# Optimization experiments

Measured on AMD Instinct MI355X. Metric: run time of the kernel, lower is better.

The kernel has to match this reference:

```python
import jax, jax.numpy as jnp
import numpy as np

B, T_PREFIX, C_IN = 8, 6144, 8
OUT_LEN, OUT_C = 2048, 8
AUX_DIM = 16
D_MODEL, D_STATE, HEADDIM, EXPAND = 256, 32, 64, 2
D_INNER = EXPAND * D_MODEL            # 512
NHEADS = D_INNER // HEADDIM           # 8
CONV_DIM = D_INNER + 2 * D_STATE      # 576
D_PROJ = 2 * D_INNER + 2 * D_STATE + NHEADS  # 1096
N_LAYERS = 2
CHUNK = 64
PATCH = 16
PRECONV_K = 5
DCONV_K = 4


def setup_inputs() -> dict:
    key = jax.random.key(0)
    ks = iter(jax.random.split(key, 64))
    def rn(shape, s=0.02):
        return s * jax.random.normal(next(ks), shape, jnp.float32)
    inp = dict(
        x_prefix=jax.random.normal(next(ks), (B, T_PREFIX, C_IN), jnp.float32),
        y_aux=jax.random.normal(next(ks), (B, AUX_DIM), jnp.float32),
        pre_conv_w=rn((D_MODEL, C_IN, PRECONV_K), 0.1),
        pre_conv_b=rn((D_MODEL,)),
        patch_w=rn((D_MODEL, D_MODEL, PATCH), 0.05),
        patch_b=rn((D_MODEL,)),
        mask_token=rn((D_MODEL,)),
        aux_w=rn((AUX_DIM, D_MODEL), 0.1),
        aux_b=rn((D_MODEL,)),
        patch_out_w=rn((2 * D_MODEL, OUT_C * PATCH), 0.05),
        patch_out_b=rn((OUT_C * PATCH,)),
    )
    for d in ('fwd', 'bwd'):
        inp[f'{d}_norm_w'] = jnp.ones((N_LAYERS, D_MODEL), jnp.float32)
        inp[f'{d}_inproj'] = rn((N_LAYERS, D_MODEL, D_PROJ), 0.05)
        inp[f'{d}_conv_w'] = rn((N_LAYERS, CONV_DIM, DCONV_K), 0.2)
        inp[f'{d}_conv_b'] = rn((N_LAYERS, CONV_DIM))
        inp[f'{d}_dtbias'] = rn((N_LAYERS, NHEADS), 0.5)
        inp[f'{d}_Alog'] = jnp.tile(jnp.log(jnp.arange(1, NHEADS + 1, dtype=jnp.float32)), (N_LAYERS, 1))
        inp[f'{d}_D'] = jnp.ones((N_LAYERS, NHEADS), jnp.float32)
        inp[f'{d}_gnorm'] = jnp.ones((N_LAYERS, D_INNER), jnp.float32)
        inp[f'{d}_outproj'] = rn((N_LAYERS, D_INNER, D_MODEL), 0.05)
    return inp


def rmsnorm(x, w, eps=1e-5):
    return x * jax.lax.rsqrt(jnp.mean(x * x, axis=-1, keepdims=True) + eps) * w


def conv1d(x, w, b, stride, pad):  # x: [B,C,T], w: [O,I,K]
    y = jax.lax.conv_general_dilated(x, w, (stride,), [(pad, pad)],
                                     dimension_numbers=('NCH', 'OIH', 'NCH'))
    return y + b[None, :, None]


def mamba_block(u, inproj, conv_w, conv_b, dtbias, Alog, Dp, gnorm_w, outproj):
    # Mamba-2/SSD style block: in_proj -> z | xBC | dt, causal depthwise conv,
    # selective scan with per-head scalar decay A, +D skip, gated RMSNorm, out_proj.
    b, T, _ = u.shape
    zxbcdt = u @ inproj                                   # [b,T,D_PROJ]
    z = zxbcdt[..., :D_INNER]
    xBC = zxbcdt[..., D_INNER:D_INNER + CONV_DIM]
    dt = jax.nn.softplus(zxbcdt[..., -NHEADS:] + dtbias)  # [b,T,H]
    # causal depthwise conv over time
    xc = jax.lax.conv_general_dilated(xBC.transpose(0, 2, 1), conv_w[:, None, :], (1,),
                                      [(DCONV_K - 1, 0)],
                                      dimension_numbers=('NCH', 'OIH', 'NCH'),
                                      feature_group_count=CONV_DIM)
    xBC = jax.nn.silu((xc + conv_b[None, :, None]).transpose(0, 2, 1))
    xs = xBC[..., :D_INNER].reshape(b, T, NHEADS, HEADDIM)  # [b,T,H,P]
    Bm = xBC[..., D_INNER:D_INNER + D_STATE]                # [b,T,N]
    Cm = xBC[..., D_INNER + D_STATE:]                       # [b,T,N]
    A = -jnp.exp(Alog)                                      # [H]

    def step(h, inps):  # h: [b,H,P,N]
        dt_t, x_t, B_t, C_t = inps
        dA = jnp.exp(dt_t * A)[:, :, None, None]
        h = h * dA + (dt_t[:, :, None] * x_t)[..., None] * B_t[:, None, None, :]
        y = jnp.einsum('bhpn,bn->bhp', h, C_t)
        return h, y

    h0 = jnp.zeros((b, NHEADS, HEADDIM, D_STATE), u.dtype)
    _, ys = jax.lax.scan(step, h0, (dt.transpose(1, 0, 2), xs.transpose(1, 0, 2, 3),
                                    Bm.transpose(1, 0, 2), Cm.transpose(1, 0, 2)))
    y = ys.transpose(1, 0, 2, 3) + Dp[None, None, :, None] * xs
    y = y.reshape(b, T, D_INNER)
    y = rmsnorm(y * jax.nn.silu(z), gnorm_w)
    return y @ outproj


def reference(x_prefix, y_aux, pre_conv_w, pre_conv_b, patch_w, patch_b, mask_token,
              aux_w, aux_b, fwd_norm_w, fwd_inproj, fwd_conv_w, fwd_conv_b, fwd_dtbias,
              fwd_Alog, fwd_D, fwd_gnorm, fwd_outproj, bwd_norm_w, bwd_inproj,
              bwd_conv_w, bwd_conv_b, bwd_dtbias, bwd_Alog, bwd_D, bwd_gnorm,
              bwd_outproj, patch_out_w, patch_out_b):
    b = x_prefix.shape[0]
    t_total = T_PREFIX + OUT_LEN
    x_full = jnp.pad(x_prefix, ((0, 0), (0, OUT_LEN), (0, 0)))        # zeros for future
    x = jax.nn.silu(conv1d(x_full.transpose(0, 2, 1), pre_conv_w, pre_conv_b, 1, PRECONV_K // 2))
    x = conv1d(x, patch_w, patch_b, PATCH, 0).transpose(0, 2, 1)      # [b, n_tokens, d_model]
    n_tokens = x.shape[1]
    # eval mode: deterministic future-patch mask, dropout is identity
    starts = jnp.arange(n_tokens) * PATCH
    mask = (starts >= T_PREFIX)[None, :, None]
    x = jnp.where(mask, mask_token[None, None, :], x)
    aux_bias = jax.nn.silu(y_aux @ aux_w + aux_b)[:, None, :]
    x = x + aux_bias
    pad_t = (-n_tokens) % CHUNK
    if pad_t:
        x = jnp.pad(x, ((0, 0), (0, pad_t), (0, 0)))
    h_f = x
    h_b = x[:, ::-1]
    for i in range(N_LAYERS):
        h_f = h_f + mamba_block(rmsnorm(h_f, fwd_norm_w[i]), fwd_inproj[i], fwd_conv_w[i],
                                fwd_conv_b[i], fwd_dtbias[i], fwd_Alog[i], fwd_D[i],
                                fwd_gnorm[i], fwd_outproj[i])
        h_b = h_b + mamba_block(rmsnorm(h_b, bwd_norm_w[i]), bwd_inproj[i], bwd_conv_w[i],
                                bwd_conv_b[i], bwd_dtbias[i], bwd_Alog[i], bwd_D[i],
                                bwd_gnorm[i], bwd_outproj[i])
    h = jnp.concatenate([h_f, h_b[:, ::-1]], axis=-1)[:, :n_tokens]   # [b,n,2*d_model]
    patch_pred = h @ patch_out_w + patch_out_b                        # [b,n,out_c*patch]
    y = patch_pred.reshape(b, n_tokens, OUT_C, PATCH).reshape(b, n_tokens * PATCH, OUT_C)
    y = y[:, :t_total, :]
    return y[:, T_PREFIX:, :]
```

## Files before the change

### kernel.cpp

```cpp
#include <hip/hip_runtime.h>
#include <hip/hip_bf16.h>
#include <math.h>

#define BSZ      8
#define TPREF    6144
#define CIN      8
#define DMODEL   256
#define DINNER   512
#define DSTATE   32
#define NHEADS   8
#define HEADDIM  64
#define CONVDIM  576
#define DPROJ    1096
#define ZXW      1088
#define NTOK     512
#define NVIS     384
#define TBWD     128
#define MFWD     (BSZ * NTOK)
#define MBWD     (BSZ * TBWD)
#define MALL     (MFWD + MBWD)

typedef float f32x4 __attribute__((ext_vector_type(4)));
typedef __bf16 bf16x8 __attribute__((ext_vector_type(8)));

// ... 28 lines not shown
        for (int i = 0; i < 2; i++) {
            int s = i * 256 + tid;
            ASYNC16(A + (size_t)(m0 + (s >> 2)) * K + kb + (s & 3) * 8, sm + s * 16);
        }
        #pragma unroll
        for (int i = 0; i < 2; i++) {
            int s = i * 256 + tid;
            ASYNC16(Bt + (size_t)(n0 + (s >> 2)) * K + kb + (s & 3) * 8, sm + 8192 + s * 16);
        }
        __syncthreads();
        bf16x8 af[4], bfr[4];
        #pragma unroll
        for (int mf = 0; mf < 4; mf++)
            af[mf] = *(const bf16x8*)(sm + (wm * 64 + mf * 16 + lm) * 64 + q * 16);
        #pragma unroll
        for (int nf = 0; nf < 4; nf++)
            bfr[nf] = *(const bf16x8*)(sm + 8192 + (wn * 64 + nf * 16 + lm) * 64 + q * 16);
        #pragma unroll
        for (int mf = 0; mf < 4; mf++)
            #pragma unroll
            for (int nf = 0; nf < 4; nf++)
                acc[mf][nf] = __builtin_amdgcn_mfma_f32_16x16x32_bf16(af[mf], bfr[nf], acc[mf][nf], 0, 0, 0);
        __syncthreads();
    }

    #pragma unroll
    for (int mf = 0; mf < 4; mf++) {
        int mbase = m0 + wm * 64 + mf * 16 + q * 4;
        #pragma unroll
        for (int nf = 0; nf < 4; nf++) {
            int n = n0 + wn * 64 + nf * 16 + lm;
            if (n < N) {
                #pragma unroll
                for (int r = 0; r < 4; r++) {
                    float v = acc[mf][nf][r];
                    if (flags & 4) {
                        v = silu_f(v + bias[n]);
                        ((__bf16*)C)[(size_t)(mbase + r) * ldc + n] = (__bf16)v;
                    } else if (flags & 16) {
                        int mm = mbase + r;
                        int bb = mm / NVIS, tk = mm - bb * NVIS;
                        atomicAdd(C + ((size_t)(bb * NTOK + tk)) * 256 + n, v);
                    } else if (flags & 2) {
                        atomicAdd(C + (size_t)(mbase + r) * ldc + n, v);
                    } else {
                        C[(size_t)(mbase + r) * ldc + n] = v;
                    }
                }
            }
        }
    }
}

__global__ __launch_bounds__(256) void final_gemm(
    const float* __restrict__ h_all, const __bf16* __restrict__ poT,
    float* __restrict__ out) {
    __shared__ __bf16 Asm_[128][40];
    __shared__ char Bsm[8192];
    int tid = threadIdx.x;
    int m0 = blockIdx.y * 128;
    int z = blockIdx.z;
    int w = tid >> 6, l = tid & 63;
    int wm = w >> 1, wn_ = w & 1, lm = l & 15, q = l >> 4;
    f32x4 acc[4][4];
    #pragma unroll
    for (int i = 0; i < 4; i++)
        #pragma unroll
        for (int j = 0; j < 4; j++) acc[i][j] = (f32x4)0.f;

    int r = tid >> 1, half = tid & 1;
    int m = m0 + r;
    int b = m >> 7, jj = m & 127;
    size_t arow = (z == 0) ? ((size_t)(b * NTOK + NVIS + jj) * 256)
                           : ((size_t)MFWD * 256 + (size_t)(b * TBWD + (TBWD - 1 - jj)) * 256);
    for (int k0 = 0; k0 < 256; k0 += 32) {
        {
            const float4* sp = (const float4*)(h_all + arow + k0 + half * 16);
            float4 v0 = sp[0], v1 = sp[1], v2 = sp[2], v3 = sp[3];
            union { uint4 u; __bf16 hh[8]; } d0, d1;
            d0.hh[0] = (__bf16)v0.x; d0.hh[1] = (__bf16)v0.y; d0.hh[2] = (__bf16)v0.z; d0.hh[3] = (__bf16)v0.w;
            d0.hh[4] = (__bf16)v1.x; d0.hh[5] = (__bf16)v1.y; d0.hh[6] = (__bf16)v1.z; d0.hh[7] = (__bf16)v1.w;
            d1.hh[0] = (__bf16)v2.x; d1.hh[1] = (__bf16)v2.y; d1.hh[2] = (__bf16)v2.z; d1.hh[3] = (__bf16)v2.w;
            d1.hh[4] = (__bf16)v3.x; d1.hh[5] = (__bf16)v3.y; d1.hh[6] = (__bf16)v3.z; d1.hh[7] = (__bf16)v3.w;
            *(uint4*)&Asm_[r][half * 16] = d0.u;
            *(uint4*)&Asm_[r][half * 16 + 8] = d1.u;
        }
        #pragma unroll
        for (int i = 0; i < 2; i++) {
            int s = i * 256 + tid;
            ASYNC16(poT + (size_t)(s >> 2) * 512 + z * 256 + k0 + (s & 3) * 8, Bsm + s * 16);
        }
        __syncthreads();
        bf16x8 af[4], bfr[4];
        #pragma unroll
        for (int mf = 0; mf < 4; mf++)
            af[mf] = *(const bf16x8*)&Asm_[wm * 64 + mf * 16 + lm][q * 8];
        #pragma unroll
        for (int nf = 0; nf < 4; nf++)
            bfr[nf] = *(const bf16x8*)(Bsm + (wn_ * 64 + nf * 16 + lm) * 64 + q * 16);
        #pragma unroll
        for (int mf = 0; mf < 4; mf++)
            #pragma unroll
            for (int nf = 0; nf < 4; nf++)
                acc[mf][nf] = __builtin_amdgcn_mfma_f32_16x16x32_bf16(af[mf], bfr[nf], acc[mf][nf], 0, 0, 0);
        __syncthreads();
    }
    #pragma unroll
    for (int mf = 0; mf < 4; mf++) {
        int mbase = m0 + wm * 64 + mf * 16 + q * 4;
        #pragma unroll
        for (int nf = 0; nf < 4; nf++) {
            int n = wn_ * 64 + nf * 16 + lm;
            #pragma unroll
            for (int rr = 0; rr < 4; rr++)
                atomicAdd(out + (size_t)(mbase + rr) * 128 + n, acc[mf][nf][rr]);
        }
    }
}

__global__ __launch_bounds__(256) void gemm_inproj(
    const __bf16* __restrict__ u, const __bf16* __restrict__ ipTf,
    const __bf16* __restrict__ ipTb, __bf16* __restrict__ zxb, float* __restrict__ dtc) {
    __shared__ char sm[16384];
    int tid = threadIdx.x;
    int m0 = blockIdx.y * 128, n0 = blockIdx.x * 128;
    const __bf16* Bt = (m0 >= MFWD) ? ipTb : ipTf;
    int w = tid >> 6, l = tid & 63;
    int wm = w >> 1, wn = w & 1, lm = l & 15, q = l >> 4;
    f32x4 acc[4][4];
    #pragma unroll
    for (int i = 0; i < 4; i++)
        #pragma unroll
        for (int j = 0; j < 4; j++) acc[i][j] = (f32x4)0.f;
    for (int k0 = 0; k0 < 256; k0 += 32) {
        #pragma unroll
        for (int i = 0; i < 2; i++) {
            int s = i * 256 + tid;
            ASYNC16(u + (size_t)(m0 + (s >> 2)) * 256 + k0 + (s & 3) * 8, sm + s * 16);
        }
        #pragma unroll
        for (int i = 0; i < 2; i++) {
            int s = i * 256 + tid;
            ASYNC16(Bt + (size_t)(n0 + (s >> 2)) * 256 + k0 + (s & 3) * 8, sm + 8192 + s * 16);
// ... 88 lines not shown
}

__global__ __launch_bounds__(256) void rmsnorm_all(
    const float* __restrict__ h, const float* __restrict__ wf,
    const float* __restrict__ wb, __bf16* __restrict__ u) {
    int row = blockIdx.x * 4 + (threadIdx.x >> 6);
    int lane = threadIdx.x & 63;
    const float* w = (row >= MFWD) ? wb : wf;
    float4 v = ((const float4*)(h + (size_t)row * 256))[lane];
    float ss = v.x * v.x + v.y * v.y + v.z * v.z + v.w * v.w;
    #pragma unroll
    for (int off = 32; off >= 1; off >>= 1) ss += __shfl_xor(ss, off);
    float rs = rsqrtf(ss * (1.f / 256.f) + 1e-5f);
    float4 wv = ((const float4*)w)[lane];
    __bf16 o4[4] = {(__bf16)(v.x * rs * wv.x), (__bf16)(v.y * rs * wv.y),
                    (__bf16)(v.z * rs * wv.z), (__bf16)(v.w * rs * wv.w)};
    *(uint2*)(u + (size_t)row * 256 + lane * 4) = *(uint2*)o4;
}

__global__ __launch_bounds__(256) void gatednorm_all(
    const __bf16* __restrict__ ysD, const __bf16* __restrict__ zxb,
    const float* __restrict__ gwf, const float* __restrict__ gwb,
    __bf16* __restrict__ y2) {
    int row = blockIdx.x * 4 + (threadIdx.x >> 6);
    int lane = threadIdx.x & 63;
    const float* gw = (row >= MFWD) ? gwb : gwf;
    union { uint4 u; __bf16 hh[8]; } yv, zv;
    yv.u = *(const uint4*)(ysD + (size_t)row * 512 + lane * 8);
    zv.u = *(const uint4*)(zxb + (size_t)row * ZXW + lane * 8);
    float g[8];
    #pragma unroll
    for (int j = 0; j < 8; j++) g[j] = (float)yv.hh[j] * silu_f((float)zv.hh[j]);
    float ss = 0.f;
    #pragma unroll
    for (int j = 0; j < 8; j++) ss += g[j] * g[j];
    #pragma unroll
    for (int off = 32; off >= 1; off >>= 1) ss += __shfl_xor(ss, off);
    float rs = rsqrtf(ss * (1.f / 512.f) + 1e-5f);
    const float4* gr = (const float4*)(gw + lane * 8);
    float4 g0 = gr[0], g1 = gr[1];
    union { uint4 u; __bf16 hh[8]; } d;
    d.hh[0] = (__bf16)(g[0] * rs * g0.x); d.hh[1] = (__bf16)(g[1] * rs * g0.y);
    d.hh[2] = (__bf16)(g[2] * rs * g0.z); d.hh[3] = (__bf16)(g[3] * rs * g0.w);
    d.hh[4] = (__bf16)(g[4] * rs * g1.x); d.hh[5] = (__bf16)(g[5] * rs * g1.y);
    d.hh[6] = (__bf16)(g[6] * rs * g1.z); d.hh[7] = (__bf16)(g[7] * rs * g1.w);
    *(uint4*)(y2 + (size_t)row * 512 + lane * 8) = d.u;
}

__global__ void prep_all(const float* __restrict__ pre_conv_w, const float* __restrict__ patch_w,
                         const float* __restrict__ ip0, const float* __restrict__ ip1,
                         const float* __restrict__ op0, const float* __restrict__ op1,
                         const float* __restrict__ pow_, const float* __restrict__ pob,
                         const float* __restrict__ y_aux, const float* __restrict__ aux_w,
                         const float* __restrict__ aux_b, const float* __restrict__ xp,
                         const float* __restrict__ patch_b, const float* __restrict__ mtok,
                         __bf16* __restrict__ WpreT, __bf16* __restrict__ WtT,
                         __bf16* __restrict__ inprojT, __bf16* __restrict__ outprojT,
                         __bf16* __restrict__ poT, float* __restrict__ dout,
                         __bf16* __restrict__ Aim, float* __restrict__ h_all) {
    __shared__ float tile[32][33];
    int bx = blockIdx.x, tid = threadIdx.x;
    int tx = tid & 31, ty = tid >> 5;
    if (bx < 256) {
        int o = bx, c = tid;
        float f[16];
        const float4* s = (const float4*)(patch_w + (size_t)o * 4096 + c * 16);
        #pragma unroll
        for (int j = 0; j < 4; j++) *(float4*)&f[j * 4] = s[j];
        #pragma unroll
        for (int k = 0; k < 16; k++)
            WtT[(size_t)o * 4096 + k * 256 + c] = (__bf16)f[k];
        return;
    }
    bx -= 256;
    if (bx < 1152) {
        int seg = bx / 288, rem = bx % 288;
        int n0 = (rem / 8) * 32, k0 = (rem % 8) * 32;
        const float* src = (seg < 2 ? ip0 : ip1) + (size_t)(seg & 1) * 256 * DPROJ;
        #pragma unroll
        for (int j = 0; j < 4; j++) {
            int r = ty + j * 8;
            int n = n0 + tx;
            tile[r][tx] = (n < DPROJ) ? src[(size_t)(k0 + r) * DPROJ + n] : 0.f;
        }
        __syncthreads();
        __bf16* dst = inprojT + (size_t)seg * 1152 * 256;
        #pragma unroll
        for (int j = 0; j < 4; j++) {
            int r = ty + j * 8;
            dst[(size_t)(n0 + r) * 256 + k0 + tx] = (__bf16)tile[tx][r];
        }
        return;
    }
    bx -= 1152;
    if (bx < 512) {
        int s = bx / 128, rem = bx % 128;
        int n0 = (rem / 16) * 32, k0 = (rem % 16) * 32;
        const float* src = (s < 2 ? op0 : op1) + (size_t)(s & 1) * DINNER * DMODEL;
        #pragma unroll
        for (int j = 0; j < 4; j++) {
            int r = ty + j * 8;
            tile[r][tx] = src[(size_t)(k0 + r) * 256 + n0 + tx];
        }
        __syncthreads();
        __bf16* dst = outprojT + (size_t)s * 256 * 512;
        #pragma unroll
        for (int j = 0; j < 4; j++) {
            int r = ty + j * 8;
            dst[(size_t)(n0 + r) * 512 + k0 + tx] = (__bf16)tile[tx][r];
        }
        return;
    }
    bx -= 512;
    if (bx < 64) {
        int n0 = (bx / 16) * 32, k0 = (bx % 16) * 32;
        #pragma unroll
        for (int j = 0; j < 4; j++) {
            int r = ty + j * 8;
            tile[r][tx] = pow_[(size_t)(k0 + r) * 128 + n0 + tx];
        }
        __syncthreads();
        #pragma unroll
        for (int j = 0; j < 4; j++) {
            int r = ty + j * 8;
            poT[(size_t)(n0 + r) * 512 + k0 + tx] = (__bf16)tile[tx][r];
        }
        return;
    }
    bx -= 64;
    if (bx < 64) {
        int idx = bx * 256 + tid;
        int o = idx >> 6, kk = idx & 63;
        WpreT[idx] = (kk < 40) ? (__bf16)pre_conv_w[o * 40 + kk] : (__bf16)0.f;
        return;
    }
    bx -= 64;
    if (bx < 512) {
        int idx = bx * 256 + tid;
        dout[idx] = pob[idx & 127];
        return;
    }
    bx -= 512;
    if (bx < 192) {
        int m = bx * 256 + tid;
        int t = m % TPREF, b = m / TPREF;
        __bf16 d[64];
        #pragma unroll
        for (int k = 0; k < 5; k++) {
            int tt = t - 2 + k;
            bool ok = (tt >= 0) && (tt < TPREF);
            const float* s = xp + ((size_t)b * TPREF + tt) * 8;
            #pragma unroll
            for (int i = 0; i < 8; i++)
                d[i * 5 + k] = ok ? (__bf16)s[i] : (__bf16)0.f;
        }
        #pragma unroll
        for (int j = 40; j < 64; j++) d[j] = (__bf16)0.f;
        uint4* o = (uint4*)(Aim + (size_t)m * 64);
        #pragma unroll
        for (int k = 0; k < 8; k++) o[k] = ((const uint4*)d)[k];
        return;
    }
    bx -= 192;
    {
        int row = bx, o = tid;
        int b; bool masked;
        if (row < MFWD) { b = row >> 9; int tok = row & 511; masked = (tok >= NVIS); }
        else { b = (row - MFWD) >> 7; masked = true; }
        float acc = aux_b[o];
        #pragma unroll
        for (int i = 0; i < 16; i++) acc += y_aux[b * 16 + i] * aux_w[i * 256 + o];
        float v = (masked ? mtok[o] : patch_b[o]) + silu_f(acc);
        h_all[(size_t)row * 256 + o] = v;
    }
}

__global__ __launch_bounds__(256) void dwconv2_kernel(
    const __bf16* __restrict__ zxb, const float* __restrict__ cwf, const float* __restrict__ cbf,
    const float* __restrict__ cwb, const float* __restrict__ cbb,
    __bf16* __restrict__ XtF, __bf16* __restrict__ XtB,
    __bf16* __restrict__ BCF, __bf16* __restrict__ BCB) {
    int cg = blockIdx.x;
    int id = blockIdx.y;
    int b, t0, T; size_t rowbase;
    const float *cw, *cb; __bf16 *Xt, *BC;
    if (id < 64) { b = id >> 3; t0 = (id & 7) * 64; T = NTOK; rowbase = (size_t)b * NTOK;
                   cw = cwf; cb = cbf; Xt = XtF; BC = BCF; }
    else { int i2 = id - 64; b = i2 >> 1; t0 = (i2 & 1) * 64; T = TBWD;
           rowbase = (size_t)MFWD + (size_t)b * TBWD; cw = cwb; cb = cbb; Xt = XtB; BC = BCB; }
    int c0 = cg * 64;
    __shared__ float xs[67][65];
    int lane = threadIdx.x & 63, grp = threadIdx.x >> 6;
    for (int r = grp; r < 67; r += 4) {
        int t = t0 - 3 + r;
        xs[r][lane] = (t >= 0) ? (float)zxb[(rowbase + t) * ZXW + DINNER + c0 + lane] : 0.f;
    }
    __syncthreads();
    if (cg < 8) {
        int t = lane;
        #pragma unroll
        for (int ci = grp; ci < 64; ci += 4) {
            int c = c0 + ci;
            float acc = cb[c];
            #pragma unroll
            for (int k = 0; k < 4; k++) acc += cw[c * 4 + k] * xs[t + k][ci];
            Xt[((size_t)((b * 8 + cg) * 64 + ci)) * T + t0 + t] = (__bf16)silu_f(acc);
        }
    } else {
        int c = lane;
        #pragma unroll
        for (int ti = grp; ti < 64; ti += 4) {
            float acc = cb[c0 + c];
            #pragma unroll
            for (int k = 0; k < 4; k++) acc += cw[(c0 + c) * 4 + k] * xs[ti + k][c];
            BC[((size_t)(b * T + t0 + ti)) * 64 + c] = (__bf16)silu_f(acc);
        }
    }
}

__global__ __launch_bounds__(64) void scan_local(
    const __bf16* __restrict__ XtF, const __bf16* __restrict__ XtB,
    const __bf16* __restrict__ BCF, const __bf16* __restrict__ BCB,
    const float* __restrict__ dtc,
    const float* __restrict__ dtbf, const float* __restrict__ dtbb,
    const float* __restrict__ Alogf, const float* __restrict__ Alogb,
    const float* __restrict__ Dpf, const float* __restrict__ Dpb,
    __bf16* __restrict__ ysD,
    __bf16* __restrict__ ChatF, __bf16* __restrict__ ChatB,
    float* __restrict__ dSF, float* __restrict__ dSB,
    float* __restrict__ DcsF, float* __restrict__ DcsB, int layer) {
    int id = blockIdx.x, hd = blockIdx.y;
    int b, c, T, NC; size_t rowbase;
    const __bf16 *Xt, *BC; __bf16* Chat; float *dS, *Dcs;
    const float *dtb, *Alog, *Dp;
    if (id < 64) { b = id >> 3; c = id & 7; T = NTOK; NC = 8; rowbase = (size_t)b * NTOK;
                   Xt = XtF; BC = BCF; Chat = ChatF; dS = dSF; Dcs = DcsF;
                   dtb = dtbf; Alog = Alogf; Dp = Dpf; }
    else { int i2 = id - 64; b = i2 >> 1; c = i2 & 1; T = TBWD; NC = 2;
           rowbase = (size_t)MFWD + (size_t)b * TBWD;
           Xt = XtB; BC = BCB; Chat = ChatB; dS = dSB; Dcs = DcsB;
           dtb = dtbb; Alog = Alogb; Dp = Dpb; }
    bool skipY = (layer == 1) && (id < 64) && (c < 6);
    int bh = b * 8 + hd;
    int t0 = c * 64;
    int lane = threadIdx.x;
    int lm = lane & 15, q = lane >> 4;
    float A = -expf(Alog[hd]);
    float Dh = Dp[hd];

    __shared__ char smem[23552];
    __bf16 (*Xl)[72]  = (__bf16(*)[72])(smem);
    __bf16 (*BCl)[72] = (__bf16(*)[72])(smem + 9216);
    __bf16 (*Pl)[72]  = (__bf16(*)[72])(smem + 9216);
    __bf16 (*Wbl)[72] = (__bf16(*)[72])(smem + 18432);
    float* lcs = (float*)(smem + 23040);
    float* dts = (float*)(smem + 23296);

    const uint4* xg = (const uint4*)(Xt + (size_t)(bh * 64 + lane) * T + t0);
    const uint4* bg = (const uint4*)(BC + ((size_t)(b * T + t0 + lane)) * 64);
    uint4 xv[8], bv[8];
    #pragma unroll
    for (int k = 0; k < 8; k++) { xv[k] = xg[k]; bv[k] = bg[k]; }
    float xdt = dtc[(rowbase + t0 + lane) * 8 + hd] + dtb[hd];
    float dtv = (xdt > 20.f) ? xdt : log1pf(expf(xdt));
    #pragma unroll
    for (int k = 0; k < 8; k++) {
        *(uint4*)&Xl[lane][k * 8] = xv[k];
        if (!skipY) *(uint4*)&BCl[lane][k * 8] = bv[k];
    }
    float lc = A * dtv;
    #pragma unroll
    for (int off = 1; off < 64; off <<= 1) {
        float o = __shfl_up(lc, off);
        if (lane >= off) lc += o;
    }
    lcs[lane] = lc; dts[lane] = dtv;
    float lc63 = __shfl(lc, 63);
    float wj = expf(lc63 - lc) * dtv;
    float eli = expf(lc);
    float Dc = expf(lc63);
    if (lane == 0) Dcs[bh * NC + c] = Dc;
    if (!skipY) {
        __bf16* co = Chat + ((size_t)(bh * NC + c) * 64 + lane) * 32;
        #pragma unroll
        for (int k = 0; k < 4; k++) {
            union { uint4 u; __bf16 h[8]; } s; s.u = bv[4 + k];
            union { uint4 u; __bf16 h[8]; } d;
            #pragma unroll
            for (int j = 0; j < 8; j++) d.h[j] = (__bf16)(eli * (float)s.h[j]);
            *(uint4*)(co + k * 8) = d.u;
        }
    }
    #pragma unroll
    for (int k = 0; k < 4; k++) {
        union { uint4 u; __bf16 h[8]; } s; s.u = bv[k];
        #pragma unroll
        for (int j = 0; j < 8; j++) Wbl[k * 8 + j][lane] = (__bf16)(wj * (float)s.h[j]);
    }
    __syncthreads();

    bf16x8 xf0[4], xf1[4];
    if (!skipY) {
        bf16x8 cfr[4], bfr[4];
        #pragma unroll
        for (int t4 = 0; t4 < 4; t4++) {
            cfr[t4] = *(const bf16x8*)&BCl[t4 * 16 + lm][32 + q * 8];
            bfr[t4] = *(const bf16x8*)&BCl[t4 * 16 + lm][q * 8];
        }
        #pragma unroll
        for (int ti = 0; ti < 4; ti++) {
            float lci[4];
            #pragma unroll
            for (int r = 0; r < 4; r++) lci[r] = lcs[ti * 16 + q * 4 + r];
            #pragma unroll
            for (int tj = 0; tj < 4; tj++) {
                if (tj > ti) {
                    #pragma unroll
                    for (int r = 0; r < 4; r++) Pl[ti * 16 + q * 4 + r][tj * 16 + lm] = (__bf16)0.f;
                    continue;
                }
                f32x4 g = __builtin_amdgcn_mfma_f32_16x16x32_bf16(cfr[ti], bfr[tj], (f32x4)0.f, 0, 0, 0);
                int j = tj * 16 + lm;
                float lcj = lcs[j], dtj = dts[j];
                #pragma unroll
                for (int r = 0; r < 4; r++) {
                    int i = ti * 16 + q * 4 + r;
                    float v = (j <= i) ? g[r] * expf(lci[r] - lcj) * dtj : 0.f;
                    if (j == i) v += Dh;
                    Pl[i][j] = (__bf16)v;
                }
            }
        }
        __syncthreads();

// ... 88 lines not shown
    int w = tid >> 6, l = tid & 63, lm = l & 15, q = l >> 4;
    for (int c = cmin + w; c < NC; c += 4) {
        int t0 = c * 64;
        const __bf16* Cb = Chat + (size_t)(bh * NC + c) * 2048;
        bf16x8 cf[4], sf[4];
        #pragma unroll
        for (int t4 = 0; t4 < 4; t4++) {
            cf[t4] = *(const bf16x8*)(Cb + (t4 * 16 + lm) * 32 + q * 8);
            sf[t4] = *(const bf16x8*)&Spl[c][t4 * 16 + lm][q * 8];
        }
        #pragma unroll
        for (int ti = 0; ti < 4; ti++) {
            #pragma unroll
            for (int tp = 0; tp < 4; tp++) {
                f32x4 y = __builtin_amdgcn_mfma_f32_16x16x32_bf16(cf[ti], sf[tp], (f32x4)0.f, 0, 0, 0);
                #pragma unroll
                for (int r = 0; r < 4; r++) {
                    int i = ti * 16 + q * 4 + r;
                    size_t idx = (rowbase + t0 + i) * DINNER + hd * 64 + tp * 16 + lm;
                    ysD[idx] = (__bf16)((float)ysD[idx] + y[r]);
                }
            }
        }
    }
}

extern "C" void kernel_launch(void* const* d_in, const int* in_sizes, int n_in,
                              void* d_out, int out_size, void* d_ws, size_t ws_size,
                              hipStream_t stream) {
    const float* x_prefix    = (const float*)d_in[0];
    const float* y_aux       = (const float*)d_in[1];
    const float* pre_conv_w  = (const float*)d_in[2];
    const float* pre_conv_b  = (const float*)d_in[3];
    const float* patch_w     = (const float*)d_in[4];
    const float* patch_b     = (const float*)d_in[5];
    const float* mask_token  = (const float*)d_in[6];
    const float* aux_w       = (const float*)d_in[7];
    const float* aux_b       = (const float*)d_in[8];
    const float* patch_out_w = (const float*)d_in[9];
    const float* patch_out_b = (const float*)d_in[10];
    const float* w_norm[2]   = {(const float*)d_in[11], (const float*)d_in[20]};
    const float* w_inproj[2] = {(const float*)d_in[12], (const float*)d_in[21]};
    const float* w_convw[2]  = {(const float*)d_in[13], (const float*)d_in[22]};
    const float* w_convb[2]  = {(const float*)d_in[14], (const float*)d_in[23]};
    const float* w_dtb[2]    = {(const float*)d_in[15], (const float*)d_in[24]};
    const float* w_alog[2]   = {(const float*)d_in[16], (const float*)d_in[25]};
    const float* w_D[2]      = {(const float*)d_in[17], (const float*)d_in[26]};
    const float* w_gnorm[2]  = {(const float*)d_in[18], (const float*)d_in[27]};
    const float* w_outproj[2]= {(const float*)d_in[19], (const float*)d_in[28]};

    char* p = (char*)d_ws;
    auto alloc = [&](size_t bytes) { char* r = p; p += (bytes + 255) & ~255ULL; return r; };
    __bf16* A_patch  = (__bf16*)alloc((size_t)3072 * 4096 * 2);
    __bf16* Aim      = (__bf16*)alloc((size_t)BSZ * TPREF * 64 * 2);
    __bf16* WpreT    = (__bf16*)alloc((size_t)256 * 64 * 2);
    __bf16* WtT      = (__bf16*)alloc((size_t)256 * 4096 * 2);
    __bf16* inprojT  = (__bf16*)alloc((size_t)4 * 1152 * 256 * 2);
    __bf16* outprojT = (__bf16*)alloc((size_t)4 * 256 * 512 * 2);
    __bf16* poT      = (__bf16*)alloc((size_t)128 * 512 * 2);
    float*  h_all    = (float*)alloc((size_t)MALL * 256 * 4);
    __bf16* u        = (__bf16*)alloc((size_t)MALL * 256 * 2);
    __bf16* zxb      = (__bf16*)alloc((size_t)MALL * ZXW * 2);
    float*  dtc      = (float*)alloc((size_t)MALL * 8 * 4);
    __bf16* XtF      = (__bf16*)alloc((size_t)64 * 64 * NTOK * 2);
    __bf16* XtB      = (__bf16*)alloc((size_t)64 * 64 * TBWD * 2);
    __bf16* BCF      = (__bf16*)alloc((size_t)BSZ * NTOK * 64 * 2);
    __bf16* BCB      = (__bf16*)alloc((size_t)BSZ * TBWD * 64 * 2);
    __bf16* ysD      = (__bf16*)alloc((size_t)MALL * DINNER * 2);
    __bf16* y2       = (__bf16*)alloc((size_t)MALL * DINNER * 2);
    __bf16* ChatF    = (__bf16*)alloc((size_t)64 * 8 * 2048 * 2);
    __bf16* ChatB    = (__bf16*)alloc((size_t)64 * 2 * 2048 * 2);
    float*  dSF      = (float*)alloc((size_t)64 * 8 * 2048 * 4);
    float*  dSB      = (float*)alloc((size_t)64 * 2 * 2048 * 4);
    float*  DcsF     = (float*)alloc((size_t)64 * 8 * 4);
    float*  DcsB     = (float*)alloc((size_t)64 * 2 * 4);

    prep_all<<<256 + 1152 + 512 + 64 + 64 + 512 + 192 + MALL, 256, 0, stream>>>(
        pre_conv_w, patch_w, w_inproj[0], w_inproj[1], w_outproj[0], w_outproj[1],
        patch_out_w, patch_out_b, y_aux, aux_w, aux_b, x_prefix, patch_b, mask_token,
        WpreT, WtT, inprojT, outprojT, poT, (float*)d_out, Aim, h_all);
    gemm_mfma<<<dim3(2, (BSZ * TPREF) / 128, 1), 256, 0, stream>>>(
        Aim, WpreT, (float*)A_patch, pre_conv_b, 256, 64, 256, 4);
    gemm_mfma<<<dim3(2, 24, 8), 256, 0, stream>>>(
        A_patch, WtT, h_all, nullptr, 256, 4096, 256, 16);

    for (int i = 0; i < 2; i++) {
        const __bf16* ipTf = inprojT + (size_t)(0 * 2 + i) * 1152 * 256;
        const __bf16* ipTb = inprojT + (size_t)(1 * 2 + i) * 1152 * 256;
        const __bf16* opTf = outprojT + (size_t)(0 * 2 + i) * 256 * 512;
        const __bf16* opTb = outprojT + (size_t)(1 * 2 + i) * 256 * 512;
        rmsnorm_all<<<MALL / 4, 256, 0, stream>>>(h_all, w_norm[0] + i * 256, w_norm[1] + i * 256, u);
        gemm_inproj<<<dim3(9, MALL / 128), 256, 0, stream>>>(u, ipTf, ipTb, zxb, dtc);
        dwconv2_kernel<<<dim3(9, 80), 256, 0, stream>>>(
            zxb, w_convw[0] + i * CONVDIM * 4, w_convb[0] + i * CONVDIM,
            w_convw[1] + i * CONVDIM * 4, w_convb[1] + i * CONVDIM,
            XtF, XtB, BCF, BCB);
        scan_local<<<dim3(80, NHEADS), 64, 0, stream>>>(
            XtF, XtB, BCF, BCB, dtc,
            w_dtb[0] + i * 8, w_dtb[1] + i * 8,
            w_alog[0] + i * 8, w_alog[1] + i * 8,
            w_D[0] + i * 8, w_D[1] + i * 8,
            ysD, ChatF, ChatB, dSF, dSB, DcsF, DcsB, i);
        scan_tail<<<128, 256, 0, stream>>>(dSF, dSB, DcsF, DcsB, ChatF, ChatB, ysD, i);
        gatednorm_all<<<MALL / 4, 256, 0, stream>>>(
            ysD, zxb, w_gnorm[0] + i * DINNER, w_gnorm[1] + i * DINNER, y2);
        int oy = (i == 0) ? (MALL / 128) : 16;
        gemm_outproj<<<dim3(2, oy), 256, 0, stream>>>(y2, opTf, opTb, h_all, i);
    }

    final_gemm<<<dim3(1, 8, 2), 256, 0, stream>>>(h_all, poT, (float*)d_out);
}
```

Measured before the change: 338.2 us.

## Fuse im2col into preconv GEMM, depthwise conv into scan, split final GEMM K

```diff
diff --git a/kernel.cpp b/kernel.cpp
--- a/kernel.cpp
+++ b/kernel.cpp
@@ -104,6 +104,78 @@
     }
 }
 
+__global__ __launch_bounds__(256) void preconv_gemm(
+    const float* __restrict__ xp, const __bf16* __restrict__ WpreT,
+    const float* __restrict__ bias, __bf16* __restrict__ Apatch) {
+    __shared__ char sm[32768];
+    int tid = threadIdx.x;
+    int m0 = blockIdx.y * 128, n0 = blockIdx.x * 128;
+    int w = tid >> 6, l = tid & 63;
+    int wm = w >> 1, wn = w & 1, lm = l & 15, q = l >> 4;
+
+    #pragma unroll
+    for (int i = 0; i < 4; i++) {
+        int s = i * 256 + tid;
+        int kh = s >> 9, row = (s & 511) >> 2, within = s & 3;
+        ASYNC16(WpreT + (size_t)(n0 + row) * 64 + kh * 32 + within * 8, sm + 16384 + s * 16);
+    }
+    if (tid < 128) {
+        int m = m0 + tid;
+        int b = m / TPREF, t = m - b * TPREF;
+        __bf16 d[64];
+        #pragma unroll
+        for (int j = 40; j < 64; j++) d[j] = (__bf16)0.f;
+        #pragma unroll
+        for (int k = 0; k < 5; k++) {
+            int tt = t - 2 + k;
+            bool ok = (tt >= 0) && (tt < TPREF);
+            const float* s = xp + ((size_t)b * TPREF + tt) * 8;
+            #pragma unroll
+            for (int i = 0; i < 8; i++)
+                d[i * 5 + k] = ok ? (__bf16)s[i] : (__bf16)0.f;
+        }
+        uint4* o0 = (uint4*)(sm + tid * 64);
+        uint4* o1 = (uint4*)(sm + 8192 + tid * 64);
+        #pragma unroll
+        for (int k = 0; k < 4; k++) { o0[k] = ((const uint4*)d)[k]; o1[k] = ((const uint4*)d)[4 + k]; }
+    }
+    __syncthreads();
+
+    f32x4 acc[4][4];
+    #pragma unroll
+    for (int i = 0; i < 4; i++)
+        #pragma unroll
+        for (int j = 0; j < 4; j++) acc[i][j] = (f32x4)0.f;
+    #pragma unroll
+    for (int kh = 0; kh < 2; kh++) {
+        bf16x8 af[4], bfr[4];
+        #pragma unroll
+        for (int mf = 0; mf < 4; mf++)
+            af[mf] = *(const bf16x8*)(sm + kh * 8192 + (wm * 64 + mf * 16 + lm) * 64 + q * 16);
+        #pragma unroll
+        for (int nf = 0; nf < 4; nf++)
+            bfr[nf] = *(const bf16x8*)(sm + 16384 + kh * 8192 + (wn * 64 + nf * 16 + lm) * 64 + q * 16);
+        #pragma unroll
+        for (int mf = 0; mf < 4; mf++)
+            #pragma unroll
+            for (int nf = 0; nf < 4; nf++)
+                acc[mf][nf] = __builtin_amdgcn_mfma_f32_16x16x32_bf16(af[mf], bfr[nf], acc[mf][nf], 0, 0, 0);
+    }
+    #pragma unroll
+    for (int mf = 0; mf < 4; mf++) {
+        int mbase = m0 + wm * 64 + mf * 16 + q * 4;
+        #pragma unroll
+        for (int nf = 0; nf < 4; nf++) {
+            int n = n0 + wn * 64 + nf * 16 + lm;
+            #pragma unroll
+            for (int r = 0; r < 4; r++) {
+                float v = silu_f(acc[mf][nf][r] + bias[n]);
+                Apatch[(size_t)(mbase + r) * 256 + n] = (__bf16)v;
+            }
+        }
+    }
+}
+
 __global__ __launch_bounds__(256) void final_gemm(
     const float* __restrict__ h_all, const __bf16* __restrict__ poT,
     float* __restrict__ out) {
@@ -112,6 +184,8 @@
     int tid = threadIdx.x;
     int m0 = blockIdx.y * 128;
     int z = blockIdx.z;
+    int dir = z >> 1, kh = z & 1;
+    int koff = kh * 128;
     int w = tid >> 6, l = tid & 63;
     int wm = w >> 1, wn_ = w & 1, lm = l & 15, q = l >> 4;
     f32x4 acc[4][4];
@@ -123,11 +197,11 @@
     int r = tid >> 1, half = tid & 1;
     int m = m0 + r;
     int b = m >> 7, jj = m & 127;
-    size_t arow = (z == 0) ? ((size_t)(b * NTOK + NVIS + jj) * 256)
-                           : ((size_t)MFWD * 256 + (size_t)(b * TBWD + (TBWD - 1 - jj)) * 256);
-    for (int k0 = 0; k0 < 256; k0 += 32) {
+    size_t arow = (dir == 0) ? ((size_t)(b * NTOK + NVIS + jj) * 256)
+                             : ((size_t)MFWD * 256 + (size_t)(b * TBWD + (TBWD - 1 - jj)) * 256);
+    for (int k0 = 0; k0 < 128; k0 += 32) {
         {
-            const float4* sp = (const float4*)(h_all + arow + k0 + half * 16);
+            const float4* sp = (const float4*)(h_all + arow + koff + k0 + half * 16);
             float4 v0 = sp[0], v1 = sp[1], v2 = sp[2], v3 = sp[3];
             union { uint4 u; __bf16 hh[8]; } d0, d1;
             d0.hh[0] = (__bf16)v0.x; d0.hh[1] = (__bf16)v0.y; d0.hh[2] = (__bf16)v0.z; d0.hh[3] = (__bf16)v0.w;
@@ -140,7 +214,7 @@
         #pragma unroll
         for (int i = 0; i < 2; i++) {
             int s = i * 256 + tid;
-            ASYNC16(poT + (size_t)(s >> 2) * 512 + z * 256 + k0 + (s & 3) * 8, Bsm + s * 16);
+            ASYNC16(poT + (size_t)(s >> 2) * 512 + dir * 256 + koff + k0 + (s & 3) * 8, Bsm + s * 16);
         }
         __syncthreads();
         bf16x8 af[4], bfr[4];
@@ -335,12 +409,12 @@
                          const float* __restrict__ op0, const float* __restrict__ op1,
                          const float* __restrict__ pow_, const float* __restrict__ pob,
                          const float* __restrict__ y_aux, const float* __restrict__ aux_w,
-                         const float* __restrict__ aux_b, const float* __restrict__ xp,
+                         const float* __restrict__ aux_b,
                          const float* __restrict__ patch_b, const float* __restrict__ mtok,
                          __bf16* __restrict__ WpreT, __bf16* __restrict__ WtT,
                          __bf16* __restrict__ inprojT, __bf16* __restrict__ outprojT,
                          __bf16* __restrict__ poT, float* __restrict__ dout,
-                         __bf16* __restrict__ Aim, float* __restrict__ h_all) {
+                         float* __restrict__ h_all) {
     __shared__ float tile[32][33];
     int bx = blockIdx.x, tid = threadIdx.x;
     int tx = tid & 31, ty = tid >> 5;
@@ -424,27 +498,6 @@
         return;
     }
     bx -= 512;
-    if (bx < 192) {
-        int m = bx * 256 + tid;
-        int t = m % TPREF, b = m / TPREF;
-        __bf16 d[64];
-        #pragma unroll
-        for (int k = 0; k < 5; k++) {
-            int tt = t - 2 + k;
-            bool ok = (tt >= 0) && (tt < TPREF);
-            const float* s = xp + ((size_t)b * TPREF + tt) * 8;
-            #pragma unroll
-            for (int i = 0; i < 8; i++)
-                d[i * 5 + k] = ok ? (__bf16)s[i] : (__bf16)0.f;
-        }
-        #pragma unroll
-        for (int j = 40; j < 64; j++) d[j] = (__bf16)0.f;
-        uint4* o = (uint4*)(Aim + (size_t)m * 64);
-        #pragma unroll
-        for (int k = 0; k < 8; k++) o[k] = ((const uint4*)d)[k];
-        return;
-    }
-    bx -= 192;
     {
         int row = bx, o = tid;
         int b; bool masked;
@@ -458,52 +511,10 @@
     }
 }
 
-__global__ __launch_bounds__(256) void dwconv2_kernel(
-    const __bf16* __restrict__ zxb, const float* __restrict__ cwf, const float* __restrict__ cbf,
+__global__ __launch_bounds__(64) void scan_local(
+    const __bf16* __restrict__ zxb,
+    const float* __restrict__ cwf, const float* __restrict__ cbf,
     const float* __restrict__ cwb, const float* __restrict__ cbb,
-    __bf16* __restrict__ XtF, __bf16* __restrict__ XtB,
-    __bf16* __restrict__ BCF, __bf16* __restrict__ BCB) {
-    int cg = blockIdx.x;
-    int id = blockIdx.y;
-    int b, t0, T; size_t rowbase;
-    const float *cw, *cb; __bf16 *Xt, *BC;
-    if (id < 64) { b = id >> 3; t0 = (id & 7) * 64; T = NTOK; rowbase = (size_t)b * NTOK;
-                   cw = cwf; cb = cbf; Xt = XtF; BC = BCF; }
-    else { int i2 = id - 64; b = i2 >> 1; t0 = (i2 & 1) * 64; T = TBWD;
-           rowbase = (size_t)MFWD + (size_t)b * TBWD; cw = cwb; cb = cbb; Xt = XtB; BC = BCB; }
-    int c0 = cg * 64;
-    __shared__ float xs[67][65];
-    int lane = threadIdx.x & 63, grp = threadIdx.x >> 6;
-    for (int r = grp; r < 67; r += 4) {
-        int t = t0 - 3 + r;
-        xs[r][lane] = (t >= 0) ? (float)zxb[(rowbase + t) * ZXW + DINNER + c0 + lane] : 0.f;
-    }
-    __syncthreads();
-    if (cg < 8) {
-        int t = lane;
-        #pragma unroll
-        for (int ci = grp; ci < 64; ci += 4) {
-            int c = c0 + ci;
-            float acc = cb[c];
-            #pragma unroll
-            for (int k = 0; k < 4; k++) acc += cw[c * 4 + k] * xs[t + k][ci];
-            Xt[((size_t)((b * 8 + cg) * 64 + ci)) * T + t0 + t] = (__bf16)silu_f(acc);
-        }
-    } else {
-        int c = lane;
-        #pragma unroll
-        for (int ti = grp; ti < 64; ti += 4) {
-            float acc = cb[c0 + c];
-            #pragma unroll
-            for (int k = 0; k < 4; k++) acc += cw[(c0 + c) * 4 + k] * xs[ti + k][c];
-            BC[((size_t)(b * T + t0 + ti)) * 64 + c] = (__bf16)silu_f(acc);
-        }
-    }
-}
-
-__global__ __launch_bounds__(64) void scan_local(
-    const __bf16* __restrict__ XtF, const __bf16* __restrict__ XtB,
-    const __bf16* __restrict__ BCF, const __bf16* __restrict__ BCB,
     const float* __restrict__ dtc,
     const float* __restrict__ dtbf, const float* __restrict__ dtbb,
     const float* __restrict__ Alogf, const float* __restrict__ Alogb,
@@ -514,15 +525,15 @@
     float* __restrict__ DcsF, float* __restrict__ DcsB, int layer) {
     int id = blockIdx.x, hd = blockIdx.y;
     int b, c, T, NC; size_t rowbase;
-    const __bf16 *Xt, *BC; __bf16* Chat; float *dS, *Dcs;
-    const float *dtb, *Alog, *Dp;
+    __bf16* Chat; float *dS, *Dcs;
+    const float *dtb, *Alog, *Dp, *cw, *cb;
     if (id < 64) { b = id >> 3; c = id & 7; T = NTOK; NC = 8; rowbase = (size_t)b * NTOK;
-                   Xt = XtF; BC = BCF; Chat = ChatF; dS = dSF; Dcs = DcsF;
-                   dtb = dtbf; Alog = Alogf; Dp = Dpf; }
+                   Chat = ChatF; dS = dSF; Dcs = DcsF;
+                   dtb = dtbf; Alog = Alogf; Dp = Dpf; cw = cwf; cb = cbf; }
     else { int i2 = id - 64; b = i2 >> 1; c = i2 & 1; T = TBWD; NC = 2;
            rowbase = (size_t)MFWD + (size_t)b * TBWD;
-           Xt = XtB; BC = BCB; Chat = ChatB; dS = dSB; Dcs = DcsB;
-           dtb = dtbb; Alog = Alogb; Dp = Dpb; }
+           Chat = ChatB; dS = dSB; Dcs = DcsB;
+           dtb = dtbb; Alog = Alogb; Dp = Dpb; cw = cwb; cb = cbb; }
     bool skipY = (layer == 1) && (id < 64) && (c < 6);
     int bh = b * 8 + hd;
     int t0 = c * 64;
@@ -531,26 +542,60 @@
     float A = -expf(Alog[hd]);
     float Dh = Dp[hd];
 
-    __shared__ char smem[23552];
+    __shared__ char smem[32256];
     __bf16 (*Xl)[72]  = (__bf16(*)[72])(smem);
     __bf16 (*BCl)[72] = (__bf16(*)[72])(smem + 9216);
     __bf16 (*Pl)[72]  = (__bf16(*)[72])(smem + 9216);
     __bf16 (*Wbl)[72] = (__bf16(*)[72])(smem + 18432);
     float* lcs = (float*)(smem + 23040);
     float* dts = (float*)(smem + 23296);
-
-    const uint4* xg = (const uint4*)(Xt + (size_t)(bh * 64 + lane) * T + t0);
-    const uint4* bg = (const uint4*)(BC + ((size_t)(b * T + t0 + lane)) * 64);
-    uint4 xv[8], bv[8];
-    #pragma unroll
-    for (int k = 0; k < 8; k++) { xv[k] = xg[k]; bv[k] = bg[k]; }
+    __bf16 (*raw)[64] = (__bf16(*)[64])(smem + 23552);
+
+    for (int r = 0; r < 67; r++) {
+        int t = t0 - 3 + r;
+        raw[r][lane] = (t >= 0)
+            ? zxb[(rowbase + t) * (size_t)ZXW + DINNER + hd * 64 + lane] : (__bf16)0.f;
+    }
+    __syncthreads();
+    {
+        int cX = hd * 64 + lane;
+        float w0 = cw[cX * 4], w1 = cw[cX * 4 + 1], w2 = cw[cX * 4 + 2], w3 = cw[cX * 4 + 3];
+        float cbv = cb[cX];
+        float a0 = (float)raw[0][lane], a1 = (float)raw[1][lane], a2 = (float)raw[2][lane];
+        union { uint4 u; __bf16 h[8]; } pk;
+        #pragma unroll
+        for (int t = 0; t < 64; t++) {
+            float a3 = (float)raw[t + 3][lane];
+            float acc = cbv + w0 * a0 + w1 * a1 + w2 * a2 + w3 * a3;
+            pk.h[t & 7] = (__bf16)silu_f(acc);
+            if ((t & 7) == 7) *(uint4*)&Xl[lane][t - 7] = pk.u;
+            a0 = a1; a1 = a2; a2 = a3;
+        }
+    }
+    __syncthreads();
+    for (int r = 0; r < 67; r++) {
+        int t = t0 - 3 + r;
+        raw[r][lane] = (t >= 0)
+            ? zxb[(rowbase + t) * (size_t)ZXW + 1024 + lane] : (__bf16)0.f;
+    }
+    __syncthreads();
+    {
+        int cc = 512 + lane;
+        float w0 = cw[cc * 4], w1 = cw[cc * 4 + 1], w2 = cw[cc * 4 + 2], w3 = cw[cc * 4 + 3];
+        float cbv = cb[cc];
+        float a0 = (float)raw[0][lane], a1 = (float)raw[1][lane], a2 = (float)raw[2][lane];
+        #pragma unroll
+        for (int t = 0; t < 64; t++) {
+            float a3 = (float)raw[t + 3][lane];
+            float acc = cbv + w0 * a0 + w1 * a1 + w2 * a2 + w3 * a3;
+            BCl[t][lane] = (__bf16)silu_f(acc);
+            a0 = a1; a1 = a2; a2 = a3;
+        }
+    }
+    __syncthreads();
+
     float xdt = dtc[(rowbase + t0 + lane) * 8 + hd] + dtb[hd];
     float dtv = (xdt > 20.f) ? xdt : log1pf(expf(xdt));
-    #pragma unroll
-    for (int k = 0; k < 8; k++) {
-        *(uint4*)&Xl[lane][k * 8] = xv[k];
-        if (!skipY) *(uint4*)&BCl[lane][k * 8] = bv[k];
-    }
     float lc = A * dtv;
     #pragma unroll
     for (int off = 1; off < 64; off <<= 1) {
@@ -563,6 +608,11 @@
     float eli = expf(lc);
     float Dc = expf(lc63);
     if (lane == 0) Dcs[bh * NC + c] = Dc;
+
+    uint4 bv[8];
+    #pragma unroll
+    for (int k = 0; k < 8; k++) bv[k] = *(const uint4*)&BCl[lane][k * 8];
+
     if (!skipY) {
         __bf16* co = Chat + ((size_t)(bh * NC + c) * 64 + lane) * 32;
         #pragma unroll
@@ -757,7 +807,6 @@
     char* p = (char*)d_ws;
     auto alloc = [&](size_t bytes) { char* r = p; p += (bytes + 255) & ~255ULL; return r; };
     __bf16* A_patch  = (__bf16*)alloc((size_t)3072 * 4096 * 2);
-    __bf16* Aim      = (__bf16*)alloc((size_t)BSZ * TPREF * 64 * 2);
     __bf16* WpreT    = (__bf16*)alloc((size_t)256 * 64 * 2);
     __bf16* WtT      = (__bf16*)alloc((size_t)256 * 4096 * 2);
     __bf16* inprojT  = (__bf16*)alloc((size_t)4 * 1152 * 256 * 2);
@@ -767,10 +816,6 @@
     __bf16* u        = (__bf16*)alloc((size_t)MALL * 256 * 2);
     __bf16* zxb      = (__bf16*)alloc((size_t)MALL * ZXW * 2);
     float*  dtc      = (float*)alloc((size_t)MALL * 8 * 4);
-    __bf16* XtF      = (__bf16*)alloc((size_t)64 * 64 * NTOK * 2);
-    __bf16* XtB      = (__bf16*)alloc((size_t)64 * 64 * TBWD * 2);
-    __bf16* BCF      = (__bf16*)alloc((size_t)BSZ * NTOK * 64 * 2);
-    __bf16* BCB      = (__bf16*)alloc((size_t)BSZ * TBWD * 64 * 2);
     __bf16* ysD      = (__bf16*)alloc((size_t)MALL * DINNER * 2);
     __bf16* y2       = (__bf16*)alloc((size_t)MALL * DINNER * 2);
     __bf16* ChatF    = (__bf16*)alloc((size_t)64 * 8 * 2048 * 2);
@@ -780,12 +825,12 @@
     float*  DcsF     = (float*)alloc((size_t)64 * 8 * 4);
     float*  DcsB     = (float*)alloc((size_t)64 * 2 * 4);
 
-    prep_all<<<256 + 1152 + 512 + 64 + 64 + 512 + 192 + MALL, 256, 0, stream>>>(
+    prep_all<<<256 + 1152 + 512 + 64 + 64 + 512 + MALL, 256, 0, stream>>>(
         pre_conv_w, patch_w, w_inproj[0], w_inproj[1], w_outproj[0], w_outproj[1],
-        patch_out_w, patch_out_b, y_aux, aux_w, aux_b, x_prefix, patch_b, mask_token,
-        WpreT, WtT, inprojT, outprojT, poT, (float*)d_out, Aim, h_all);
-    gemm_mfma<<<dim3(2, (BSZ * TPREF) / 128, 1), 256, 0, stream>>>(
-        Aim, WpreT, (float*)A_patch, pre_conv_b, 256, 64, 256, 4);
+        patch_out_w, patch_out_b, y_aux, aux_w, aux_b, patch_b, mask_token,
+        WpreT, WtT, inprojT, outprojT, poT, (float*)d_out, h_all);
+    preconv_gemm<<<dim3(2, (BSZ * TPREF) / 128), 256, 0, stream>>>(
+        x_prefix, WpreT, pre_conv_b, A_patch);
     gemm_mfma<<<dim3(2, 24, 8), 256, 0, stream>>>(
         A_patch, WtT, h_all, nullptr, 256, 4096, 256, 16);
 
@@ -796,12 +841,11 @@
         const __bf16* opTb = outprojT + (size_t)(1 * 2 + i) * 256 * 512;
         rmsnorm_all<<<MALL / 4, 256, 0, stream>>>(h_all, w_norm[0] + i * 256, w_norm[1] + i * 256, u);
         gemm_inproj<<<dim3(9, MALL / 128), 256, 0, stream>>>(u, ipTf, ipTb, zxb, dtc);
-        dwconv2_kernel<<<dim3(9, 80), 256, 0, stream>>>(
-            zxb, w_convw[0] + i * CONVDIM * 4, w_convb[0] + i * CONVDIM,
+        scan_local<<<dim3(80, NHEADS), 64, 0, stream>>>(
+            zxb,
+            w_convw[0] + i * CONVDIM * 4, w_convb[0] + i * CONVDIM,
             w_convw[1] + i * CONVDIM * 4, w_convb[1] + i * CONVDIM,
-            XtF, XtB, BCF, BCB);
-        scan_local<<<dim3(80, NHEADS), 64, 0, stream>>>(
-            XtF, XtB, BCF, BCB, dtc,
+            dtc,
             w_dtb[0] + i * 8, w_dtb[1] + i * 8,
             w_alog[0] + i * 8, w_alog[1] + i * 8,
             w_D[0] + i * 8, w_D[1] + i * 8,
@@ -813,5 +857,5 @@
         gemm_outproj<<<dim3(2, oy), 256, 0, stream>>>(y2, opTf, opTb, h_all, i);
     }
 
-    final_gemm<<<dim3(1, 8, 2), 256, 0, stream>>>(h_all, poT, (float*)d_out);
-}
+    final_gemm<<<dim3(1, 8, 4), 256, 0, stream>>>(h_all, poT, (float*)d_out);
+}
```

After: 380.2 us. 12.4% more time.

## Fuse im2col into pre-conv GEMM and split final GEMM along K

Applied to the files above, without the earlier changes.

```diff
diff --git a/kernel.cpp b/kernel.cpp
--- a/kernel.cpp
+++ b/kernel.cpp
@@ -104,6 +104,78 @@
     }
 }
 
+__global__ __launch_bounds__(256) void preconv_gemm(
+    const float* __restrict__ xp, const __bf16* __restrict__ WpreT,
+    const float* __restrict__ bias, __bf16* __restrict__ Apatch) {
+    __shared__ char sm[32768];
+    int tid = threadIdx.x;
+    int m0 = blockIdx.y * 128, n0 = blockIdx.x * 128;
+    int w = tid >> 6, l = tid & 63;
+    int wm = w >> 1, wn = w & 1, lm = l & 15, q = l >> 4;
+
+    #pragma unroll
+    for (int i = 0; i < 4; i++) {
+        int s = i * 256 + tid;
+        int kh = s >> 9, row = (s & 511) >> 2, within = s & 3;
+        ASYNC16(WpreT + (size_t)(n0 + row) * 64 + kh * 32 + within * 8, sm + 16384 + s * 16);
+    }
+    if (tid < 128) {
+        int m = m0 + tid;
+        int b = m / TPREF, t = m - b * TPREF;
+        __bf16 d[64];
+        #pragma unroll
+        for (int j = 40; j < 64; j++) d[j] = (__bf16)0.f;
+        #pragma unroll
+        for (int k = 0; k < 5; k++) {
+            int tt = t - 2 + k;
+            bool ok = (tt >= 0) && (tt < TPREF);
+            const float* s = xp + ((size_t)b * TPREF + tt) * 8;
+            #pragma unroll
+            for (int i = 0; i < 8; i++)
+                d[i * 5 + k] = ok ? (__bf16)s[i] : (__bf16)0.f;
+        }
+        uint4* o0 = (uint4*)(sm + tid * 64);
+        uint4* o1 = (uint4*)(sm + 8192 + tid * 64);
+        #pragma unroll
+        for (int k = 0; k < 4; k++) { o0[k] = ((const uint4*)d)[k]; o1[k] = ((const uint4*)d)[4 + k]; }
+    }
+    __syncthreads();
+
+    f32x4 acc[4][4];
+    #pragma unroll
+    for (int i = 0; i < 4; i++)
+        #pragma unroll
+        for (int j = 0; j < 4; j++) acc[i][j] = (f32x4)0.f;
+    #pragma unroll
+    for (int kh = 0; kh < 2; kh++) {
+        bf16x8 af[4], bfr[4];
+        #pragma unroll
+        for (int mf = 0; mf < 4; mf++)
+            af[mf] = *(const bf16x8*)(sm + kh * 8192 + (wm * 64 + mf * 16 + lm) * 64 + q * 16);
+        #pragma unroll
+        for (int nf = 0; nf < 4; nf++)
+            bfr[nf] = *(const bf16x8*)(sm + 16384 + kh * 8192 + (wn * 64 + nf * 16 + lm) * 64 + q * 16);
+        #pragma unroll
+        for (int mf = 0; mf < 4; mf++)
+            #pragma unroll
+            for (int nf = 0; nf < 4; nf++)
+                acc[mf][nf] = __builtin_amdgcn_mfma_f32_16x16x32_bf16(af[mf], bfr[nf], acc[mf][nf], 0, 0, 0);
+    }
+    #pragma unroll
+    for (int mf = 0; mf < 4; mf++) {
+        int mbase = m0 + wm * 64 + mf * 16 + q * 4;
+        #pragma unroll
+        for (int nf = 0; nf < 4; nf++) {
+            int n = n0 + wn * 64 + nf * 16 + lm;
+            #pragma unroll
+            for (int r = 0; r < 4; r++) {
+                float v = silu_f(acc[mf][nf][r] + bias[n]);
+                Apatch[(size_t)(mbase + r) * 256 + n] = (__bf16)v;
+            }
+        }
+    }
+}
+
 __global__ __launch_bounds__(256) void final_gemm(
     const float* __restrict__ h_all, const __bf16* __restrict__ poT,
     float* __restrict__ out) {
@@ -112,6 +184,8 @@
     int tid = threadIdx.x;
     int m0 = blockIdx.y * 128;
     int z = blockIdx.z;
+    int dir = z >> 1, kh = z & 1;
+    int koff = kh * 128;
     int w = tid >> 6, l = tid & 63;
     int wm = w >> 1, wn_ = w & 1, lm = l & 15, q = l >> 4;
     f32x4 acc[4][4];
@@ -123,11 +197,11 @@
     int r = tid >> 1, half = tid & 1;
     int m = m0 + r;
     int b = m >> 7, jj = m & 127;
-    size_t arow = (z == 0) ? ((size_t)(b * NTOK + NVIS + jj) * 256)
-                           : ((size_t)MFWD * 256 + (size_t)(b * TBWD + (TBWD - 1 - jj)) * 256);
-    for (int k0 = 0; k0 < 256; k0 += 32) {
+    size_t arow = (dir == 0) ? ((size_t)(b * NTOK + NVIS + jj) * 256)
+                             : ((size_t)MFWD * 256 + (size_t)(b * TBWD + (TBWD - 1 - jj)) * 256);
+    for (int k0 = 0; k0 < 128; k0 += 32) {
         {
-            const float4* sp = (const float4*)(h_all + arow + k0 + half * 16);
+            const float4* sp = (const float4*)(h_all + arow + koff + k0 + half * 16);
             float4 v0 = sp[0], v1 = sp[1], v2 = sp[2], v3 = sp[3];
             union { uint4 u; __bf16 hh[8]; } d0, d1;
             d0.hh[0] = (__bf16)v0.x; d0.hh[1] = (__bf16)v0.y; d0.hh[2] = (__bf16)v0.z; d0.hh[3] = (__bf16)v0.w;
@@ -140,7 +214,7 @@
         #pragma unroll
         for (int i = 0; i < 2; i++) {
             int s = i * 256 + tid;
-            ASYNC16(poT + (size_t)(s >> 2) * 512 + z * 256 + k0 + (s & 3) * 8, Bsm + s * 16);
+            ASYNC16(poT + (size_t)(s >> 2) * 512 + dir * 256 + koff + k0 + (s & 3) * 8, Bsm + s * 16);
         }
         __syncthreads();
         bf16x8 af[4], bfr[4];
@@ -335,12 +409,12 @@
                          const float* __restrict__ op0, const float* __restrict__ op1,
                          const float* __restrict__ pow_, const float* __restrict__ pob,
                          const float* __restrict__ y_aux, const float* __restrict__ aux_w,
-                         const float* __restrict__ aux_b, const float* __restrict__ xp,
+                         const float* __restrict__ aux_b,
                          const float* __restrict__ patch_b, const float* __restrict__ mtok,
                          __bf16* __restrict__ WpreT, __bf16* __restrict__ WtT,
                          __bf16* __restrict__ inprojT, __bf16* __restrict__ outprojT,
                          __bf16* __restrict__ poT, float* __restrict__ dout,
-                         __bf16* __restrict__ Aim, float* __restrict__ h_all) {
+                         float* __restrict__ h_all) {
     __shared__ float tile[32][33];
     int bx = blockIdx.x, tid = threadIdx.x;
     int tx = tid & 31, ty = tid >> 5;
@@ -424,27 +498,6 @@
         return;
     }
     bx -= 512;
-    if (bx < 192) {
-        int m = bx * 256 + tid;
-        int t = m % TPREF, b = m / TPREF;
-        __bf16 d[64];
-        #pragma unroll
-        for (int k = 0; k < 5; k++) {
-            int tt = t - 2 + k;
-            bool ok = (tt >= 0) && (tt < TPREF);
-            const float* s = xp + ((size_t)b * TPREF + tt) * 8;
-            #pragma unroll
-            for (int i = 0; i < 8; i++)
-                d[i * 5 + k] = ok ? (__bf16)s[i] : (__bf16)0.f;
-        }
-        #pragma unroll
-        for (int j = 40; j < 64; j++) d[j] = (__bf16)0.f;
-        uint4* o = (uint4*)(Aim + (size_t)m * 64);
-        #pragma unroll
-        for (int k = 0; k < 8; k++) o[k] = ((const uint4*)d)[k];
-        return;
-    }
-    bx -= 192;
     {
         int row = bx, o = tid;
         int b; bool masked;
@@ -757,7 +810,6 @@
     char* p = (char*)d_ws;
     auto alloc = [&](size_t bytes) { char* r = p; p += (bytes + 255) & ~255ULL; return r; };
     __bf16* A_patch  = (__bf16*)alloc((size_t)3072 * 4096 * 2);
-    __bf16* Aim      = (__bf16*)alloc((size_t)BSZ * TPREF * 64 * 2);
     __bf16* WpreT    = (__bf16*)alloc((size_t)256 * 64 * 2);
     __bf16* WtT      = (__bf16*)alloc((size_t)256 * 4096 * 2);
     __bf16* inprojT  = (__bf16*)alloc((size_t)4 * 1152 * 256 * 2);
@@ -780,12 +832,12 @@
     float*  DcsF     = (float*)alloc((size_t)64 * 8 * 4);
     float*  DcsB     = (float*)alloc((size_t)64 * 2 * 4);
 
-    prep_all<<<256 + 1152 + 512 + 64 + 64 + 512 + 192 + MALL, 256, 0, stream>>>(
+    prep_all<<<256 + 1152 + 512 + 64 + 64 + 512 + MALL, 256, 0, stream>>>(
         pre_conv_w, patch_w, w_inproj[0], w_inproj[1], w_outproj[0], w_outproj[1],
-        patch_out_w, patch_out_b, y_aux, aux_w, aux_b, x_prefix, patch_b, mask_token,
-        WpreT, WtT, inprojT, outprojT, poT, (float*)d_out, Aim, h_all);
-    gemm_mfma<<<dim3(2, (BSZ * TPREF) / 128, 1), 256, 0, stream>>>(
-        Aim, WpreT, (float*)A_patch, pre_conv_b, 256, 64, 256, 4);
+        patch_out_w, patch_out_b, y_aux, aux_w, aux_b, patch_b, mask_token,
+        WpreT, WtT, inprojT, outprojT, poT, (float*)d_out, h_all);
+    preconv_gemm<<<dim3(2, (BSZ * TPREF) / 128), 256, 0, stream>>>(
+        x_prefix, WpreT, pre_conv_b, A_patch);
     gemm_mfma<<<dim3(2, 24, 8), 256, 0, stream>>>(
         A_patch, WtT, h_all, nullptr, 256, 4096, 256, 16);
 
@@ -813,5 +865,5 @@
         gemm_outproj<<<dim3(2, oy), 256, 0, stream>>>(y2, opTf, opTb, h_all, i);
     }
 
-    final_gemm<<<dim3(1, 8, 2), 256, 0, stream>>>(h_all, poT, (float*)d_out);
-}
+    final_gemm<<<dim3(1, 8, 4), 256, 0, stream>>>(h_all, poT, (float*)d_out);
+}
```

Result: faster. 325.0 us (-3.9%).
